# Performance work log

Measured on AMD Instinct MI355X. Metric: run time of the kernel, lower is better.

The kernel has to match this reference:

```python
import jax, jax.numpy as jnp
import numpy as np

# Flax nn.LSTMCell math: gates i,f,g,o; input dense has no bias, hidden dense has bias.
# We fuse the four gate projections into single [D,4H] / [H,4H] matrices in order (i,f,g,o).

def _lstm_layer(x, Wx, Wh, b):
    # x: [B,T,D], Wx: [D,4H], Wh: [H,4H], b: [4H]
    B = x.shape[0]
    H = Wh.shape[0]
    # Precompute input projections for the whole sequence (one big GEMM).
    xW = jnp.einsum('btd,dg->btg', x, Wx) + b  # [B,T,4H]

    def step(carry, xw_t):
        c, h = carry
        z = xw_t + h @ Wh  # [B,4H]
        i, f, g, o = jnp.split(z, 4, axis=-1)
        i = jax.nn.sigmoid(i)
        f = jax.nn.sigmoid(f)
        g = jnp.tanh(g)
        o = jax.nn.sigmoid(o)
        c = f * c + i * g
        h = o * jnp.tanh(c)
        return (c, h), h

    init = (jnp.zeros((B, H), x.dtype), jnp.zeros((B, H), x.dtype))
    _, ys = jax.lax.scan(step, init, jnp.swapaxes(xW, 0, 1))  # scan over T
    return jnp.swapaxes(ys, 0, 1)  # [B,T,H]


def setup_inputs() -> dict:
    key = jax.random.key(0)
    ks = jax.random.split(key, 7)
    B, T, D, H = 64, 512, 512, 1024
    s = lambda fan_in: 1.0 / np.sqrt(fan_in)
    x = jax.random.normal(ks[0], (B, T, D), dtype=jnp.float32)
    Wx0 = jax.random.normal(ks[1], (D, 4 * H), dtype=jnp.float32) * s(D)
    Wh0 = jax.random.normal(ks[2], (H, 4 * H), dtype=jnp.float32) * s(H)
    b0 = jnp.zeros((4 * H,), dtype=jnp.float32)
    Wx1 = jax.random.normal(ks[3], (H, 4 * H), dtype=jnp.float32) * s(H)
    Wh1 = jax.random.normal(ks[4], (H, 4 * H), dtype=jnp.float32) * s(H)
    b1 = jnp.zeros((4 * H,), dtype=jnp.float32)
    return {"x": x, "Wx0": Wx0, "Wh0": Wh0, "b0": b0, "Wx1": Wx1, "Wh1": Wh1, "b1": b1}


def reference(x, Wx0, Wh0, b0, Wx1, Wh1, b1):
    h1 = _lstm_layer(x, Wx0, Wh0, b0)
    h2 = _lstm_layer(h1, Wx1, Wh1, b1)
    return h2
```

## Files before the change

### kernel.cpp

```cpp
#include <hip/hip_runtime.h>

typedef __attribute__((ext_vector_type(8))) short short8;
typedef __attribute__((ext_vector_type(4))) float f32x4;

#define WS_XB     0ull
#define WS_W0T    33554432ull
#define WS_W1T    46137344ull
#define WS_RING0  62914560ull
#define WS_RING1  67108864ull
#define WS_BAR    71303168ull
#define SLOT_ELEMS 65536
#define SLOT_BYTES 131072

#define ARR0(g)  ((g) * 16)
#define ARR1(g)  (128 + (g) * 16)
#define ROOT0    256
#define ROOT1    272
#define POLL0(g) (288 + (g) * 16)
#define POLL1(g) (416 + (g) * 16)

__device__ __forceinline__ unsigned short f2bf(float f) {
  unsigned u = __float_as_uint(f);
  u += 0x7FFFu + ((u >> 16) & 1u);
  return (unsigned short)(u >> 16);
}

__device__ __forceinline__ float sigm(float x) { return 1.0f / (1.0f + __expf(-x)); }

__global__ void sentinel_kernel(float* out) { out[0] = 1.0e6f; }

__global__ void convert_x_kernel(const float* __restrict__ x, unsigned short* __restrict__ xb) {
  int i = blockIdx.x * 256 + threadIdx.x;
  const float4 v = ((const float4*)x)[i];
  unsigned long long pack = (unsigned long long)f2bf(v.x)
                          | ((unsigned long long)f2bf(v.y) << 16)
                          | ((unsigned long long)f2bf(v.z) << 32)
                          | ((unsigned long long)f2bf(v.w) << 48);
  ((unsigned long long*)xb)[i] = pack;
}

__global__ void transpose_weights_kernel(const float* __restrict__ wx, const float* __restrict__ wh,
                                         unsigned short* __restrict__ dst, int Kx, int Ktot) {
  __shared__ float tile[32][33];
  const int k0 = blockIdx.x * 32, n0 = blockIdx.y * 32;
  const int tx = threadIdx.x, ty = threadIdx.y;
#pragma unroll
  for (int i = 0; i < 4; ++i) {
    int k = k0 + ty + i * 8;
    tile[ty + i * 8][tx] = (k < Kx) ? wx[(size_t)k * 4096 + n0 + tx]
                                    : wh[(size_t)(k - Kx) * 4096 + n0 + tx];
  }
  __syncthreads();
#pragma unroll
  for (int i = 0; i < 4; ++i) {
    int n = n0 + ty + i * 8;
    int r = (n & 1023) * 4 + (n >> 10);
    dst[(size_t)r * Ktot + k0 + tx] = f2bf(tile[tx][ty + i * 8]);
  }
}

template<int N1, int NBLK>
__device__ __forceinline__ void lstm_step_mfma(int a0b, int a1b,
    const unsigned short* __restrict__ r1p, const unsigned short* __restrict__ r2p,
    f32x4& acc0, f32x4& acc1)
{
  extern __shared__ unsigned short lds[];
  short8 buf[4][8];

  auto loadB = [&](int slot, int blk) {
    const unsigned short* p = (blk < N1) ? (r1p + blk * 256) : (r2p + (blk - N1) * 256);
#pragma unroll
    for (int j = 0; j < 8; ++j) buf[slot][j] = *(const short8*)(p + j * 32);
  };
  auto compute8 = [&](int slot, int kg) {
#pragma unroll
    for (int j = 0; j < 8; ++j) {
      const int ko = kg + j * 32;
      short8 a0 = *(const short8*)&lds[a0b + ko];
      short8 a1 = *(const short8*)&lds[a1b + ko];
      acc0 = __builtin_amdgcn_mfma_f32_16x16x32_bf16(a0, buf[slot][j], acc0, 0, 0, 0);
      acc1 = __builtin_amdgcn_mfma_f32_16x16x32_bf16(a1, buf[slot][j], acc1, 0, 0, 0);
    }
  };

  loadB(0, 0); loadB(1, 1); loadB(2, 2); loadB(3, 3);
  __builtin_amdgcn_sched_barrier(0);
#pragma unroll
  for (int bp = 0; bp < NBLK; ++bp) {
    compute8(bp & 3, bp * 256);
    if (bp + 4 < NBLK) loadB(bp & 3, bp + 4);
    __builtin_amdgcn_sched_barrier(0);
  }
}

__global__ void __launch_bounds__(256, 1) lstm_persistent(
    const unsigned short* __restrict__ xb,
    const unsigned short* __restrict__ w0t,
    const unsigned short* __restrict__ w1t,
    const float* __restrict__ b0v, const float* __restrict__ b1v,
    unsigned short* __restrict__ ring0, unsigned short* __restrict__ ring1,
    unsigned* __restrict__ bar,
    float* __restrict__ out)
{
  extern __shared__ unsigned short lds[];

  const int wg    = blockIdx.x;
  const int group = wg >> 7;
  const int wgl   = wg & 127;
  const int hu0   = wgl * 8;
  const int tid   = threadIdx.x;
  const int lane  = tid & 63;
  const int wid   = tid >> 6;
  const int c16   = lane & 15;
  const int row4  = lane >> 4;
  const int bb    = wid * 16 + c16;

  const int K    = group ? 2048 : 1536;
  const int KPAD = group ? 2056 : 1544;

  {
    const unsigned short* wsrc = (group ? w1t : w0t) + (size_t)(wgl * 32) * K;
    const int kv = K >> 3;
    for (int c = tid; c < 32 * kv; c += 256) {
      int r = c / kv, q = c - r * kv;
      int srcr = 8 * ((r & 15) >> 2) + 4 * (r >> 4) + (r & 3);
      *(short8*)&lds[r * KPAD + q * 8] = *(const short8*)&wsrc[(size_t)srcr * K + q * 8];
    }
  }
  __syncthreads();

  const float* bsrc = group ? b1v : b0v;
  float bias0[4], bias1[4];
#pragma unroll
  for (int j = 0; j < 4; ++j) {
    bias0[j] = bsrc[j * 1024 + hu0 + 2 * row4];
    bias1[j] = bsrc[j * 1024 + hu0 + 2 * row4 + 1];
  }

  const int a0b = c16 * KPAD + 8 * row4;
  const int a1b = a0b + 16 * KPAD;

  const int lofs = (bb << 10) + 8 * row4;
  const unsigned short* x_cur = xb + ((size_t)bb << 18) + 8 * row4;
  unsigned* rwb0 = (unsigned*)(group ? ring1 : ring0) + (((bb << 10) + hu0) >> 1);
  float* out_base = out + ((size_t)bb << 19) + hu0 + 2 * row4;

  const int grp = wgl >> 4;
  unsigned* arrw  = bar + (group ? ARR1(grp) : ARR0(grp));
  unsigned* rootw = bar + (group ? ROOT1 : ROOT0);
  unsigned long long* pollw =
      (unsigned long long*)(bar + (group ? POLL1(grp) : POLL0(grp)));

  float cst0 = 0.0f, cst1 = 0.0f;

  auto compute_episode = [&](int s) {
    const int t = group ? (s - 1) : s;

    f32x4 acc0 = { bias0[0], bias0[1], bias0[2], bias0[3] };
    f32x4 acc1 = { bias1[0], bias1[1], bias1[2], bias1[3] };

    const unsigned short* h0rd = ring0 + ((s - 1) & 31) * SLOT_ELEMS + lofs;
    if (group == 0) {
      lstm_step_mfma<2, 6>(a0b, a1b, x_cur, h0rd, acc0, acc1);
      x_cur += 512;
    } else {
      const unsigned short* h1rd = ring1 + ((s - 2) & 31) * SLOT_ELEMS + lofs;
      lstm_step_mfma<4, 8>(a0b, a1b, h0rd, h1rd, acc0, acc1);
    }

    float hv0, hv1;
    {
      float iv = sigm(acc0[0]), fv = sigm(acc0[1]);
      float gv = tanhf(acc0[2]), ov = sigm(acc0[3]);
      cst0 = fv * cst0 + iv * gv;
      hv0 = ov * tanhf(cst0);
    }
    {
      float iv = sigm(acc1[0]), fv = sigm(acc1[1]);
      float gv = tanhf(acc1[2]), ov = sigm(acc1[3]);
      cst1 = fv * cst1 + iv * gv;
      hv1 = ov * tanhf(cst1);
    }
    unsigned hp  = (unsigned)f2bf(hv0) | ((unsigned)f2bf(hv1) << 16);
    unsigned hpo = __shfl_down(hp, 16);
    if ((row4 & 1) == 0) {
      unsigned long long pk = (unsigned long long)hp | ((unsigned long long)hpo << 32);
      unsigned long long* dst = (unsigned long long*)(rwb0 + (t & 31) * (SLOT_ELEMS / 2) + row4);
      (void)__hip_atomic_exchange(dst, pk, __ATOMIC_RELAXED, __HIP_MEMORY_SCOPE_AGENT);
    }
    if (group) {
      float2 o2; o2.x = hv0; o2.y = hv1;
      *(float2*)(out_base + ((size_t)t << 10)) = o2;
    }
  };

  for (int s = 0; s < 512; ++s) {
    const bool active = group ? (s >= 1) : true;
    if (active) compute_episode(s);

    __syncthreads();
    if (tid == 0) {
      unsigned old = __hip_atomic_fetch_add(arrw, 1u, __ATOMIC_RELAXED, __HIP_MEMORY_SCOPE_AGENT);
      if (old == (unsigned)(16 * s + 15)) {
        unsigned old2 = __hip_atomic_fetch_add(rootw, 1u, __ATOMIC_RELAXED, __HIP_MEMORY_SCOPE_AGENT);
        if (old2 == (unsigned)(8 * s + 7)) {
#pragma unroll
          for (int g2 = 0; g2 < 8; ++g2) {
            (void)__hip_atomic_exchange(bar + (group ? POLL1(g2) : POLL0(g2)), (unsigned)(s + 1),
                                        __ATOMIC_RELAXED, __HIP_MEMORY_SCOPE_AGENT);
            (void)__hip_atomic_exchange(bar + (group ? POLL0(g2) : POLL1(g2)) + 1, (unsigned)(s + 1),
                                        __ATOMIC_RELAXED, __HIP_MEMORY_SCOPE_AGENT);
          }
        }
      }
      const int own_tgt = s + 1;
      const int mir_tgt = group ? (s + 1) : (s - 3);
      for (;;) {
        unsigned long long v = __hip_atomic_load(pollw, __ATOMIC_RELAXED, __HIP_MEMORY_SCOPE_AGENT);
        int rel = (int)(unsigned)v;
        int mir = (int)(unsigned)(v >> 32);
        if (rel >= own_tgt && mir >= mir_tgt) break;
        __builtin_amdgcn_s_sleep(1);
      }
    }
    __syncthreads();
  }
  if (group) compute_episode(512);
}

extern "C" void kernel_launch(void* const* d_in, const int* in_sizes, int n_in,
                              void* d_out, int out_size, void* d_ws, size_t ws_size,
                              hipStream_t stream) {
  const float* x   = (const float*)d_in[0];
  const float* Wx0 = (const float*)d_in[1];
  const float* Wh0 = (const float*)d_in[2];
  const float* b0  = (const float*)d_in[3];
  const float* Wx1 = (const float*)d_in[4];
  const float* Wh1 = (const float*)d_in[5];
  const float* b1  = (const float*)d_in[6];
  float* outp = (float*)d_out;

  char* ws = (char*)d_ws;
  unsigned short* xbp   = (unsigned short*)(ws + WS_XB);
  unsigned short* w0tp  = (unsigned short*)(ws + WS_W0T);
  unsigned short* w1tp  = (unsigned short*)(ws + WS_W1T);
  unsigned short* ring0 = (unsigned short*)(ws + WS_RING0);
  unsigned short* ring1 = (unsigned short*)(ws + WS_RING1);
  unsigned*       barp  = (unsigned*)(ws + WS_BAR);

  sentinel_kernel<<<dim3(1), dim3(1), 0, stream>>>(outp);
  convert_x_kernel<<<dim3(16384), dim3(256), 0, stream>>>(x, xbp);
  transpose_weights_kernel<<<dim3(48, 128), dim3(32, 8), 0, stream>>>(Wx0, Wh0, w0tp, 512, 1536);
  transpose_weights_kernel<<<dim3(64, 128), dim3(32, 8), 0, stream>>>(Wx1, Wh1, w1tp, 1024, 2048);
  hipMemsetAsync(ring0 + 31 * SLOT_ELEMS, 0, SLOT_BYTES, stream);
  hipMemsetAsync(ring1 + 31 * SLOT_ELEMS, 0, SLOT_BYTES, stream);
  hipMemsetAsync(barp, 0, 4096, stream);

  void* kargs[] = { (void*)&xbp, (void*)&w0tp, (void*)&w1tp, (void*)&b0, (void*)&b1,
                    (void*)&ring0, (void*)&ring1, (void*)&barp, (void*)&outp };
  hipError_t e = hipLaunchCooperativeKernel((void*)lstm_persistent, dim3(256), dim3(256),
                                            kargs, 32 * 2056 * 2 , stream);
  if (e != hipSuccess) {
    lstm_persistent<<<dim3(256), dim3(256), 32 * 2056 * 2, stream>>>(
        xbp, w0tp, w1tp, b0, b1, ring0, ring1, barp, outp);
  }
}
```

Before: 4.870 ms.

## Prefetch off-critical-path operands during barrier wait in persistent LSTM

Layer 0 now loads the next timestep's input projection fragments (x) into registers before the grid barrier wait. Layer 1 first waits for layer 0's release, then loads the layer-0 hidden state for the next step while still waiting on its own barrier. Only the recurrent h operand is loaded after the barrier, so the MFMA chain begins with fewer outstanding global loads on the critical path. The cost is extra register pressure from the persistent prefetch buffer, plus an extra sync point for layer 1.

```diff
diff --git a/kernel.cpp b/kernel.cpp
--- a/kernel.cpp
+++ b/kernel.cpp
@@ -56,40 +56,6 @@
     int n = n0 + ty + i * 8;
     int r = (n & 1023) * 4 + (n >> 10);
     dst[(size_t)r * Ktot + k0 + tx] = f2bf(tile[tx][ty + i * 8]);
-  }
-}
-
-template<int N1, int NBLK>
-__device__ __forceinline__ void lstm_step_mfma(int a0b, int a1b,
-    const unsigned short* __restrict__ r1p, const unsigned short* __restrict__ r2p,
-    f32x4& acc0, f32x4& acc1)
-{
-  extern __shared__ unsigned short lds[];
-  short8 buf[4][8];
-
-  auto loadB = [&](int slot, int blk) {
-    const unsigned short* p = (blk < N1) ? (r1p + blk * 256) : (r2p + (blk - N1) * 256);
-#pragma unroll
-    for (int j = 0; j < 8; ++j) buf[slot][j] = *(const short8*)(p + j * 32);
-  };
-  auto compute8 = [&](int slot, int kg) {
-#pragma unroll
-    for (int j = 0; j < 8; ++j) {
-      const int ko = kg + j * 32;
-      short8 a0 = *(const short8*)&lds[a0b + ko];
-      short8 a1 = *(const short8*)&lds[a1b + ko];
-      acc0 = __builtin_amdgcn_mfma_f32_16x16x32_bf16(a0, buf[slot][j], acc0, 0, 0, 0);
-      acc1 = __builtin_amdgcn_mfma_f32_16x16x32_bf16(a1, buf[slot][j], acc1, 0, 0, 0);
-    }
-  };
-
-  loadB(0, 0); loadB(1, 1); loadB(2, 2); loadB(3, 3);
-  __builtin_amdgcn_sched_barrier(0);
-#pragma unroll
-  for (int bp = 0; bp < NBLK; ++bp) {
-    compute8(bp & 3, bp * 256);
-    if (bp + 4 < NBLK) loadB(bp & 3, bp + 4);
-    __builtin_amdgcn_sched_barrier(0);
   }
 }
 
@@ -141,7 +107,7 @@
   const int a1b = a0b + 16 * KPAD;
 
   const int lofs = (bb << 10) + 8 * row4;
-  const unsigned short* x_cur = xb + ((size_t)bb << 18) + 8 * row4;
+  const unsigned short* xbase = xb + ((size_t)bb << 18) + 8 * row4;
   unsigned* rwb0 = (unsigned*)(group ? ring1 : ring0) + (((bb << 10) + hu0) >> 1);
   float* out_base = out + ((size_t)bb << 19) + hu0 + 2 * row4;
 
@@ -153,19 +119,46 @@
 
   float cst0 = 0.0f, cst1 = 0.0f;
 
+  short8 pf[4][8];
+
+  auto ld8 = [&](short8* d, const unsigned short* p) {
+#pragma unroll
+    for (int j = 0; j < 8; ++j) d[j] = *(const short8*)(p + j * 32);
+  };
+
+  if (group == 0) { ld8(pf[0], xbase); ld8(pf[1], xbase + 256); }
+
   auto compute_episode = [&](int s) {
     const int t = group ? (s - 1) : s;
 
     f32x4 acc0 = { bias0[0], bias0[1], bias0[2], bias0[3] };
     f32x4 acc1 = { bias1[0], bias1[1], bias1[2], bias1[3] };
 
+    auto mfma8 = [&](const short8* b, int bp) {
+#pragma unroll
+      for (int j = 0; j < 8; ++j) {
+        const int ko = bp * 256 + j * 32;
+        short8 a0 = *(const short8*)&lds[a0b + ko];
+        short8 a1 = *(const short8*)&lds[a1b + ko];
+        acc0 = __builtin_amdgcn_mfma_f32_16x16x32_bf16(a0, b[j], acc0, 0, 0, 0);
+        acc1 = __builtin_amdgcn_mfma_f32_16x16x32_bf16(a1, b[j], acc1, 0, 0, 0);
+      }
+    };
+
     const unsigned short* h0rd = ring0 + ((s - 1) & 31) * SLOT_ELEMS + lofs;
     if (group == 0) {
-      lstm_step_mfma<2, 6>(a0b, a1b, x_cur, h0rd, acc0, acc1);
-      x_cur += 512;
+      short8 f0[8], f1[8], f2[8], f3[8];
+      ld8(f0, h0rd); ld8(f1, h0rd + 256); ld8(f2, h0rd + 512); ld8(f3, h0rd + 768);
+      __builtin_amdgcn_sched_barrier(0);
+      mfma8(pf[0], 0); mfma8(pf[1], 1);
+      mfma8(f0, 2); mfma8(f1, 3); mfma8(f2, 4); mfma8(f3, 5);
     } else {
       const unsigned short* h1rd = ring1 + ((s - 2) & 31) * SLOT_ELEMS + lofs;
-      lstm_step_mfma<4, 8>(a0b, a1b, h0rd, h1rd, acc0, acc1);
+      short8 f0[8], f1[8], f2[8], f3[8];
+      ld8(f0, h1rd); ld8(f1, h1rd + 256); ld8(f2, h1rd + 512); ld8(f3, h1rd + 768);
+      __builtin_amdgcn_sched_barrier(0);
+      mfma8(pf[0], 0); mfma8(pf[1], 1); mfma8(pf[2], 2); mfma8(pf[3], 3);
+      mfma8(f0, 4); mfma8(f1, 5); mfma8(f2, 6); mfma8(f3, 7);
     }
 
     float hv0, hv1;
@@ -213,6 +206,24 @@
           }
         }
       }
+    }
+
+    if (group) {
+      if (tid == 0) {
+        while ((int)(unsigned)(__hip_atomic_load(pollw, __ATOMIC_RELAXED,
+                 __HIP_MEMORY_SCOPE_AGENT) >> 32) < s + 1)
+          __builtin_amdgcn_s_sleep(1);
+      }
+      __syncthreads();
+      const unsigned short* h0n = ring0 + (s & 31) * SLOT_ELEMS + lofs;
+      ld8(pf[0], h0n); ld8(pf[1], h0n + 256); ld8(pf[2], h0n + 512); ld8(pf[3], h0n + 768);
+    } else if (s + 1 < 512) {
+      const unsigned short* xn = xbase + (size_t)(s + 1) * 512;
+      ld8(pf[0], xn); ld8(pf[1], xn + 256);
+    }
+    __builtin_amdgcn_sched_barrier(0);
+
+    if (tid == 0) {
       const int own_tgt = s + 1;
       const int mir_tgt = group ? (s + 1) : (s - 3);
       for (;;) {
```

After: 6.223 ms. +27.8%, slower.
